# Performance work log

Hardware: AMD Instinct MI355X
Metric: run time of the kernel (lower is better)

## Reference

```python
import jax, jax.numpy as jnp
import numpy as np

INPUT_DIM = 1024
EMBED_DIMS = 128


def setup_inputs() -> dict:
    key = jax.random.key(0)
    ks = jax.random.split(key, 7)
    s_in = 1.0 / np.sqrt(INPUT_DIM)
    x = jax.random.normal(ks[0], (4, 4096, INPUT_DIM), dtype=jnp.float32)
    Wq = jax.random.uniform(ks[1], (INPUT_DIM, EMBED_DIMS), jnp.float32, -s_in, s_in)
    bq = jax.random.uniform(ks[2], (EMBED_DIMS,), jnp.float32, -s_in, s_in)
    Wk = jax.random.uniform(ks[3], (INPUT_DIM, EMBED_DIMS), jnp.float32, -s_in, s_in)
    bk = jax.random.uniform(ks[4], (EMBED_DIMS,), jnp.float32, -s_in, s_in)
    Wv = jax.random.uniform(ks[5], (INPUT_DIM, EMBED_DIMS), jnp.float32, -s_in, s_in)
    bv = jax.random.uniform(ks[6], (EMBED_DIMS,), jnp.float32, -s_in, s_in)
    return {"x": x, "Wq": Wq, "bq": bq, "Wk": Wk, "bk": bk, "Wv": Wv, "bv": bv}


def reference(x, Wq, bq, Wk, bk, Wv, bv):
    # x: [B, L, C]
    Q = jnp.einsum('blc,cd->bld', x, Wq) + bq  # [B, L, D]
    K = jnp.einsum('blc,cd->bld', x, Wk) + bk
    V = jnp.einsum('blc,cd->bld', x, Wv) + bv
    d_k = Q.shape[-1]
    scores = jnp.einsum('bld,bmd->blm', Q, K) / jnp.sqrt(jnp.float32(d_k))  # [B, L, L]
    attn = jax.nn.softmax(scores, axis=-1)
    return jnp.einsum('blm,bmd->bld', attn, V)  # [B, L, D]
```

## Files before the change

### kernel.cpp

```cpp
#include <hip/hip_runtime.h>
#include <stdint.h>

typedef __bf16 bf16;
typedef __bf16 bf16x8 __attribute__((ext_vector_type(8)));
typedef __bf16 bf16x4 __attribute__((ext_vector_type(4)));
typedef _Float16 f16;
typedef f16 f16x8 __attribute__((ext_vector_type(8)));
typedef f16 f16x4 __attribute__((ext_vector_type(4)));
typedef float f32x4 __attribute__((ext_vector_type(4)));

#define LQ    16384
#define CDIM  1024
#define DDIM  128
#define NSPLIT 4
#define QS 0.12751741f

__global__ void prep_kernel(const float* __restrict__ Wq, const float* __restrict__ Wk,
                            const float* __restrict__ Wv, const float* __restrict__ bq,
                            const float* __restrict__ bk, const float* __restrict__ bv,
                            bf16* __restrict__ Wt, float* __restrict__ bias_all) {
  int idx = blockIdx.x * 256 + threadIdx.x;
  int p = idx >> 17;
  int rem = idx & 131071;
  int k = rem >> 7, n = rem & 127;
  const float* W = (p == 0) ? Wq : (p == 1) ? Wk : Wv;
  float s = (p == 0) ? QS : 1.0f;
  Wt[(size_t)(p * 128 + n) * CDIM + k] = (bf16)(W[rem] * s);
  if (idx < 384) {
    int pp = idx >> 7, nn = idx & 127;
    const float* b = (pp == 0) ? bq : (pp == 1) ? bk : bv;
    bias_all[idx] = b[nn] * ((pp == 0) ? QS : 1.0f);
  }
}

__global__ __launch_bounds__(256, 2) void qkv_gemm(
    const float* __restrict__ x, const bf16* __restrict__ Wt,
    const float* __restrict__ bias_all,
    bf16* __restrict__ Qw, bf16* __restrict__ Kw, f16* __restrict__ Vtw) {
  __shared__ bf16 Al[2][128 * 72];
  __shared__ bf16 Bl[2][128 * 72];
  const int t = threadIdx.x;
  const int w = t >> 6;
  const int lane = t & 63;
  const int l15 = lane & 15;
  const int quad = lane >> 4;
  const int y = blockIdx.y;
  const int m0 = blockIdx.x * 128;
  const bf16* W = Wt + (size_t)y * (DDIM * CDIM);
  const int m_off = (w & 1) * 64;
  const int n_off = (w >> 1) * 64;

  f32x4 zero4 = {0.f, 0.f, 0.f, 0.f};
  f32x4 acc[4][4];
#pragma unroll
  for (int i = 0; i < 4; i++)
#pragma unroll
    for (int j = 0; j < 4; j++) acc[i][j] = zero4;

  const int xrr = t >> 4;
  const int xc = (t & 15) << 2;
  const int wr = t >> 3;
  const int wc = (t & 7) << 3;

  float4 xa[8];
  bf16x8 wa[4];
#pragma unroll
  for (int c = 0; c < 8; c++)
    xa[c] = *(const float4*)&x[(size_t)(m0 + c * 16 + xrr) * CDIM + xc];
#pragma unroll
  for (int c = 0; c < 4; c++)
    wa[c] = *(const bf16x8*)&W[(size_t)(c * 32 + wr) * CDIM + wc];

  for (int kc = 0; kc < 16; kc++) {
    bf16* Ab = Al[kc & 1];
    bf16* Bb = Bl[kc & 1];
#pragma unroll
    for (int c = 0; c < 8; c++) {
      bf16x4 v;
      v[0] = (bf16)xa[c].x; v[1] = (bf16)xa[c].y;
      v[2] = (bf16)xa[c].z; v[3] = (bf16)xa[c].w;
      *(bf16x4*)&Ab[(c * 16 + xrr) * 72 + xc] = v;
    }
#pragma unroll
    for (int c = 0; c < 4; c++)
      *(bf16x8*)&Bb[(c * 32 + wr) * 72 + wc] = wa[c];

    const int kn = (kc < 15 ? kc + 1 : 15) * 64;
#pragma unroll
    for (int c = 0; c < 8; c++)
      xa[c] = *(const float4*)&x[(size_t)(m0 + c * 16 + xrr) * CDIM + kn + xc];
#pragma unroll
    for (int c = 0; c < 4; c++)
      wa[c] = *(const bf16x8*)&W[(size_t)(c * 32 + wr) * CDIM + kn + wc];

    __syncthreads();

#pragma unroll
    for (int ks = 0; ks < 2; ks++) {
      bf16x8 af[4], bfr[4];
#pragma unroll
      for (int mt = 0; mt < 4; mt++)
        af[mt] = *(const bf16x8*)&Ab[(m_off + mt * 16 + l15) * 72 + ks * 32 + quad * 8];
#pragma unroll
      for (int nt = 0; nt < 4; nt++)
        bfr[nt] = *(const bf16x8*)&Bb[(n_off + nt * 16 + l15) * 72 + ks * 32 + quad * 8];
#pragma unroll
      for (int mt = 0; mt < 4; mt++)
#pragma unroll
        for (int nt = 0; nt < 4; nt++)
          acc[mt][nt] = __builtin_amdgcn_mfma_f32_16x16x32_bf16(af[mt], bfr[nt], acc[mt][nt], 0, 0, 0);
    }
  }

  float bias4[4];
#pragma unroll
  for (int nt = 0; nt < 4; nt++) bias4[nt] = bias_all[y * 128 + n_off + nt * 16 + l15];

  if (y < 2) {
    bf16* outp = (y == 0) ? Qw : Kw;
#pragma unroll
    for (int mt = 0; mt < 4; mt++)
#pragma unroll
      for (int nt = 0; nt < 4; nt++) {
        int n = n_off + nt * 16 + l15;
#pragma unroll
        for (int r = 0; r < 4; r++) {
          int m = m0 + m_off + mt * 16 + quad * 4 + r;
          outp[(size_t)m * DDIM + n] = (bf16)(acc[mt][nt][r] + bias4[nt]);
        }
      }
  } else {
#pragma unroll
    for (int mt = 0; mt < 4; mt++)
#pragma unroll
      for (int nt = 0; nt < 4; nt++) {
        int n = n_off + nt * 16 + l15;
        int m = m0 + m_off + mt * 16 + quad * 4;
        f16x4 pv;
#pragma unroll
        for (int r = 0; r < 4; r++) pv[r] = (f16)(acc[mt][nt][r] + bias4[nt]);
        *(f16x4*)&Vtw[(size_t)n * LQ + m] = pv;
      }
  }
}

__global__ __launch_bounds__(256, 2) void flash_kernel(
    const bf16* __restrict__ Qw, const bf16* __restrict__ Kw, const f16* __restrict__ Vtw,
    bf16* __restrict__ Opb, float* __restrict__ lp) {
  __shared__ bf16 Kl[2][64 * 136];
  __shared__ f16  Vl[2][128 * 72];

  const int t = threadIdx.x;
  const int w = t >> 6;
  const int lane = t & 63;
  const int l15 = lane & 15;
  const int quad = lane >> 4;
  const int qb = blockIdx.x;
  const int sp = blockIdx.y;
  const int batch = qb >> 5;
  const int q0w = qb * 128 + w * 32;
  const int kv_base = batch * 4096 + sp * 1024;

  bf16x8 qf[2][4];
#pragma unroll
  for (int nq = 0; nq < 2; nq++)
#pragma unroll
    for (int ks = 0; ks < 4; ks++)
      qf[nq][ks] = *(const bf16x8*)&Qw[(size_t)(q0w + nq * 16 + l15) * DDIM + ks * 32 + quad * 8];

  f32x4 zero4 = {0.f, 0.f, 0.f, 0.f};
  f32x4 o[2][8];
#pragma unroll
  for (int nq = 0; nq < 2; nq++)
#pragma unroll
    for (int dt = 0; dt < 8; dt++) o[nq][dt] = zero4;
  f32x4 li4[2];
  li4[0] = zero4; li4[1] = zero4;

  f16x4 onef = {(f16)1.f, (f16)1.f, (f16)1.f, (f16)1.f};

  const int kr = t >> 4;
  const int kcol = (t & 15) << 3;
  const int vr = t >> 3;
  const int vcol = (t & 7) << 3;

  bf16x8 ka[4];
  f16x8 va[4];
#pragma unroll
  for (int c = 0; c < 4; c++)
    ka[c] = *(const bf16x8*)&Kw[(size_t)(kv_base + c * 16 + kr) * DDIM + kcol];
#pragma unroll
  for (int c = 0; c < 4; c++)
    va[c] = *(const f16x8*)&Vtw[(size_t)(c * 32 + vr) * LQ + kv_base + vcol];

  for (int tile = 0; tile < 16; tile++) {
    bf16* Kb = Kl[tile & 1];
    f16*  Vb = Vl[tile & 1];
#pragma unroll
    for (int c = 0; c < 4; c++)
      *(bf16x8*)&Kb[(c * 16 + kr) * 136 + kcol] = ka[c];
#pragma unroll
    for (int c = 0; c < 4; c++)
      *(f16x8*)&Vb[(c * 32 + vr) * 72 + vcol] = va[c];

    const int kvn = kv_base + (tile < 15 ? tile + 1 : 15) * 64;
#pragma unroll
    for (int c = 0; c < 4; c++)
      ka[c] = *(const bf16x8*)&Kw[(size_t)(kvn + c * 16 + kr) * DDIM + kcol];
#pragma unroll
    for (int c = 0; c < 4; c++)
      va[c] = *(const f16x8*)&Vtw[(size_t)(c * 32 + vr) * LQ + kvn + vcol];

    __syncthreads();

    f32x4 sv[4][2];
#pragma unroll
    for (int mk = 0; mk < 4; mk++)
#pragma unroll
      for (int nq = 0; nq < 2; nq++) sv[mk][nq] = zero4;
#pragma unroll
    for (int ks = 0; ks < 4; ks++) {
      bf16x8 kf[4];
#pragma unroll
      for (int mk = 0; mk < 4; mk++)
        kf[mk] = *(const bf16x8*)&Kb[(mk * 16 + l15) * 136 + ks * 32 + quad * 8];
#pragma unroll
      for (int mk = 0; mk < 4; mk++)
#pragma unroll
        for (int nq = 0; nq < 2; nq++)
          sv[mk][nq] = __builtin_amdgcn_mfma_f32_16x16x32_bf16(kf[mk], qf[nq][ks], sv[mk][nq], 0, 0, 0);
    }

#pragma unroll
    for (int mk = 0; mk < 4; mk++)
#pragma unroll
      for (int nq = 0; nq < 2; nq++)
#pragma unroll
        for (int r = 0; r < 4; r++)
          sv[mk][nq][r] = exp2f(sv[mk][nq][r]);

#pragma unroll
    for (int s = 0; s < 4; s++) {
      f16x4 pa[2];
#pragma unroll
      for (int nq = 0; nq < 2; nq++) {
        f16x4 p;
#pragma unroll
        for (int r = 0; r < 4; r++) p[r] = (f16)sv[s][nq][r];
        pa[nq] = p;
      }
#pragma unroll
      for (int dt = 0; dt < 8; dt++) {
        f16x4 vf = *(const f16x4*)&Vb[(dt * 16 + l15) * 72 + s * 16 + quad * 4];
#pragma unroll
        for (int nq = 0; nq < 2; nq++)
          o[nq][dt] = __builtin_amdgcn_mfma_f32_16x16x16f16(pa[nq], vf, o[nq][dt], 0, 0, 0);
      }
#pragma unroll
      for (int nq = 0; nq < 2; nq++)
        li4[nq] = __builtin_amdgcn_mfma_f32_16x16x16f16(pa[nq], onef, li4[nq], 0, 0, 0);
    }
  }

  const size_t po = (size_t)sp * LQ * DDIM;
#pragma unroll
  for (int nq = 0; nq < 2; nq++)
#pragma unroll
    for (int dt = 0; dt < 8; dt++)
#pragma unroll
      for (int r = 0; r < 4; r++)
        Opb[po + (size_t)(q0w + nq * 16 + quad * 4 + r) * DDIM + dt * 16 + l15] = (bf16)o[nq][dt][r];
  if (l15 == 0) {
#pragma unroll
    for (int nq = 0; nq < 2; nq++)
#pragma unroll
      for (int r = 0; r < 4; r++)
        lp[(size_t)sp * LQ + q0w + nq * 16 + quad * 4 + r] = li4[nq][r];
  }
}

__global__ void combine_kernel(const bf16* __restrict__ Opb, const float* __restrict__ lp,
                               float* __restrict__ out) {
  int idx = blockIdx.x * 256 + threadIdx.x;
  int q = idx >> 5;
  int d = (idx & 31) * 4;
  float lsum = 0.f;
  float acc[4] = {0.f, 0.f, 0.f, 0.f};
#pragma unroll
  for (int sp = 0; sp < NSPLIT; sp++) {
    lsum += lp[(size_t)sp * LQ + q];
    bf16x4 ov = *(const bf16x4*)&Opb[(size_t)sp * LQ * DDIM + (size_t)q * DDIM + d];
#pragma unroll
    for (int j = 0; j < 4; j++) acc[j] += (float)ov[j];
  }
  float inv = 1.0f / lsum;
  float4 r;
  r.x = acc[0] * inv; r.y = acc[1] * inv; r.z = acc[2] * inv; r.w = acc[3] * inv;
  *(float4*)&out[(size_t)q * DDIM + d] = r;
}

extern "C" void kernel_launch(void* const* d_in, const int* in_sizes, int n_in,
                              void* d_out, int out_size, void* d_ws, size_t ws_size,
                              hipStream_t stream) {
  const float* x  = (const float*)d_in[0];
  const float* Wq = (const float*)d_in[1];
  const float* bq = (const float*)d_in[2];
  const float* Wk = (const float*)d_in[3];
  const float* bk = (const float*)d_in[4];
  const float* Wv = (const float*)d_in[5];
  const float* bv = (const float*)d_in[6];
  char* ws = (char*)d_ws;
  bf16* Qw   = (bf16*)(ws);
  bf16* Kw   = (bf16*)(ws + ((size_t)4 << 20));
  f16*  Vtw  = (f16*)(ws + ((size_t)8 << 20));
  bf16* Wt   = (bf16*)(ws + ((size_t)12 << 20));
  float* bias_all = (float*)(ws + ((size_t)12 << 20) + 786432);
  bf16* Opb  = (bf16*)(ws + ((size_t)13 << 20));
  float* lpp = (float*)(ws + ((size_t)29 << 20));
  float* out = (float*)d_out;

  prep_kernel<<<1536, 256, 0, stream>>>(Wq, Wk, Wv, bq, bk, bv, Wt, bias_all);
  qkv_gemm<<<dim3(128, 3), 256, 0, stream>>>(x, Wt, bias_all, Qw, Kw, Vtw);
  flash_kernel<<<dim3(128, NSPLIT), 256, 0, stream>>>(Qw, Kw, Vtw, Opb, lpp);
  combine_kernel<<<2048, 256, 0, stream>>>(Opb, lpp, out);
}
```

Measured before the change: 182.8 us.

## Shrink QKV GEMM tile, read K directly from global, store partials as fp16

After: 208.1 us. 1.14x slower.

```diff
diff --git a/kernel.cpp b/kernel.cpp
--- a/kernel.cpp
+++ b/kernel.cpp
@@ -33,79 +33,76 @@
   }
 }
 
-__global__ __launch_bounds__(256, 2) void qkv_gemm(
+__global__ __launch_bounds__(256, 3) void qkv_gemm(
     const float* __restrict__ x, const bf16* __restrict__ Wt,
     const float* __restrict__ bias_all,
     bf16* __restrict__ Qw, bf16* __restrict__ Kw, f16* __restrict__ Vtw) {
-  __shared__ bf16 Al[2][128 * 72];
-  __shared__ bf16 Bl[2][128 * 72];
+  __shared__ bf16 Al[64 * 72];
+  __shared__ bf16 Bl[128 * 72];
   const int t = threadIdx.x;
   const int w = t >> 6;
   const int lane = t & 63;
   const int l15 = lane & 15;
   const int quad = lane >> 4;
   const int y = blockIdx.y;
-  const int m0 = blockIdx.x * 128;
+  const int m0 = blockIdx.x * 64;
   const bf16* W = Wt + (size_t)y * (DDIM * CDIM);
-  const int m_off = (w & 1) * 64;
+  const int m_off = (w & 1) * 32;
   const int n_off = (w >> 1) * 64;
-
-  f32x4 zero4 = {0.f, 0.f, 0.f, 0.f};
-  f32x4 acc[4][4];
-#pragma unroll
-  for (int i = 0; i < 4; i++)
-#pragma unroll
-    for (int j = 0; j < 4; j++) acc[i][j] = zero4;
-
-  const int xrr = t >> 4;
+  const int xr = t >> 4;
   const int xc = (t & 15) << 2;
   const int wr = t >> 3;
   const int wc = (t & 7) << 3;
 
-  float4 xa[8];
+  f32x4 zero4 = {0.f, 0.f, 0.f, 0.f};
+  f32x4 acc[2][4];
+#pragma unroll
+  for (int i = 0; i < 2; i++)
+#pragma unroll
+    for (int j = 0; j < 4; j++) acc[i][j] = zero4;
+
+  float4 xa[4];
   bf16x8 wa[4];
 #pragma unroll
-  for (int c = 0; c < 8; c++)
-    xa[c] = *(const float4*)&x[(size_t)(m0 + c * 16 + xrr) * CDIM + xc];
+  for (int c = 0; c < 4; c++)
+    xa[c] = *(const float4*)&x[(size_t)(m0 + c * 16 + xr) * CDIM + xc];
 #pragma unroll
   for (int c = 0; c < 4; c++)
     wa[c] = *(const bf16x8*)&W[(size_t)(c * 32 + wr) * CDIM + wc];
 
   for (int kc = 0; kc < 16; kc++) {
-    bf16* Ab = Al[kc & 1];
-    bf16* Bb = Bl[kc & 1];
-#pragma unroll
-    for (int c = 0; c < 8; c++) {
+    __syncthreads();
+#pragma unroll
+    for (int c = 0; c < 4; c++) {
       bf16x4 v;
       v[0] = (bf16)xa[c].x; v[1] = (bf16)xa[c].y;
       v[2] = (bf16)xa[c].z; v[3] = (bf16)xa[c].w;
-      *(bf16x4*)&Ab[(c * 16 + xrr) * 72 + xc] = v;
+      *(bf16x4*)&Al[(c * 16 + xr) * 72 + xc] = v;
     }
 #pragma unroll
     for (int c = 0; c < 4; c++)
-      *(bf16x8*)&Bb[(c * 32 + wr) * 72 + wc] = wa[c];
+      *(bf16x8*)&Bl[(c * 32 + wr) * 72 + wc] = wa[c];
+    __syncthreads();
 
     const int kn = (kc < 15 ? kc + 1 : 15) * 64;
 #pragma unroll
-    for (int c = 0; c < 8; c++)
-      xa[c] = *(const float4*)&x[(size_t)(m0 + c * 16 + xrr) * CDIM + kn + xc];
+    for (int c = 0; c < 4; c++)
+      xa[c] = *(const float4*)&x[(size_t)(m0 + c * 16 + xr) * CDIM + kn + xc];
 #pragma unroll
     for (int c = 0; c < 4; c++)
       wa[c] = *(const bf16x8*)&W[(size_t)(c * 32 + wr) * CDIM + kn + wc];
 
-    __syncthreads();
-
 #pragma unroll
     for (int ks = 0; ks < 2; ks++) {
-      bf16x8 af[4], bfr[4];
-#pragma unroll
-      for (int mt = 0; mt < 4; mt++)
-        af[mt] = *(const bf16x8*)&Ab[(m_off + mt * 16 + l15) * 72 + ks * 32 + quad * 8];
+      bf16x8 af[2], bfr[4];
+#pragma unroll
+      for (int mt = 0; mt < 2; mt++)
+        af[mt] = *(const bf16x8*)&Al[(m_off + mt * 16 + l15) * 72 + ks * 32 + quad * 8];
 #pragma unroll
       for (int nt = 0; nt < 4; nt++)
-        bfr[nt] = *(const bf16x8*)&Bb[(n_off + nt * 16 + l15) * 72 + ks * 32 + quad * 8];
-#pragma unroll
-      for (int mt = 0; mt < 4; mt++)
+        bfr[nt] = *(const bf16x8*)&Bl[(n_off + nt * 16 + l15) * 72 + ks * 32 + quad * 8];
+#pragma unroll
+      for (int mt = 0; mt < 2; mt++)
 #pragma unroll
         for (int nt = 0; nt < 4; nt++)
           acc[mt][nt] = __builtin_amdgcn_mfma_f32_16x16x32_bf16(af[mt], bfr[nt], acc[mt][nt], 0, 0, 0);
@@ -119,7 +116,7 @@
   if (y < 2) {
     bf16* outp = (y == 0) ? Qw : Kw;
 #pragma unroll
-    for (int mt = 0; mt < 4; mt++)
+    for (int mt = 0; mt < 2; mt++)
 #pragma unroll
       for (int nt = 0; nt < 4; nt++) {
         int n = n_off + nt * 16 + l15;
@@ -131,7 +128,7 @@
       }
   } else {
 #pragma unroll
-    for (int mt = 0; mt < 4; mt++)
+    for (int mt = 0; mt < 2; mt++)
 #pragma unroll
       for (int nt = 0; nt < 4; nt++) {
         int n = n_off + nt * 16 + l15;
@@ -146,9 +143,8 @@
 
 __global__ __launch_bounds__(256, 2) void flash_kernel(
     const bf16* __restrict__ Qw, const bf16* __restrict__ Kw, const f16* __restrict__ Vtw,
-    bf16* __restrict__ Opb, float* __restrict__ lp) {
-  __shared__ bf16 Kl[2][64 * 136];
-  __shared__ f16  Vl[2][128 * 72];
+    f16* __restrict__ Opb, float* __restrict__ lp) {
+  __shared__ f16 Vl[2][128 * 72];
 
   const int t = threadIdx.x;
   const int w = t >> 6;
@@ -179,26 +175,17 @@
 
   f16x4 onef = {(f16)1.f, (f16)1.f, (f16)1.f, (f16)1.f};
 
-  const int kr = t >> 4;
-  const int kcol = (t & 15) << 3;
   const int vr = t >> 3;
   const int vcol = (t & 7) << 3;
 
-  bf16x8 ka[4];
   f16x8 va[4];
-#pragma unroll
-  for (int c = 0; c < 4; c++)
-    ka[c] = *(const bf16x8*)&Kw[(size_t)(kv_base + c * 16 + kr) * DDIM + kcol];
 #pragma unroll
   for (int c = 0; c < 4; c++)
     va[c] = *(const f16x8*)&Vtw[(size_t)(c * 32 + vr) * LQ + kv_base + vcol];
 
   for (int tile = 0; tile < 16; tile++) {
-    bf16* Kb = Kl[tile & 1];
-    f16*  Vb = Vl[tile & 1];
-#pragma unroll
-    for (int c = 0; c < 4; c++)
-      *(bf16x8*)&Kb[(c * 16 + kr) * 136 + kcol] = ka[c];
+    const int kv0 = kv_base + tile * 64;
+    f16* Vb = Vl[tile & 1];
 #pragma unroll
     for (int c = 0; c < 4; c++)
       *(f16x8*)&Vb[(c * 32 + vr) * 72 + vcol] = va[c];
@@ -206,49 +193,34 @@
     const int kvn = kv_base + (tile < 15 ? tile + 1 : 15) * 64;
 #pragma unroll
     for (int c = 0; c < 4; c++)
-      ka[c] = *(const bf16x8*)&Kw[(size_t)(kvn + c * 16 + kr) * DDIM + kcol];
-#pragma unroll
-    for (int c = 0; c < 4; c++)
       va[c] = *(const f16x8*)&Vtw[(size_t)(c * 32 + vr) * LQ + kvn + vcol];
 
     __syncthreads();
 
-    f32x4 sv[4][2];
-#pragma unroll
-    for (int mk = 0; mk < 4; mk++)
-#pragma unroll
-      for (int nq = 0; nq < 2; nq++) sv[mk][nq] = zero4;
-#pragma unroll
-    for (int ks = 0; ks < 4; ks++) {
+#pragma unroll
+    for (int s = 0; s < 4; s++) {
       bf16x8 kf[4];
 #pragma unroll
-      for (int mk = 0; mk < 4; mk++)
-        kf[mk] = *(const bf16x8*)&Kb[(mk * 16 + l15) * 136 + ks * 32 + quad * 8];
-#pragma unroll
-      for (int mk = 0; mk < 4; mk++)
+      for (int ks = 0; ks < 4; ks++)
+        kf[ks] = *(const bf16x8*)&Kw[(size_t)(kv0 + s * 16 + l15) * DDIM + ks * 32 + quad * 8];
+
+      f32x4 sv[2];
+      sv[0] = zero4; sv[1] = zero4;
+#pragma unroll
+      for (int ks = 0; ks < 4; ks++)
 #pragma unroll
         for (int nq = 0; nq < 2; nq++)
-          sv[mk][nq] = __builtin_amdgcn_mfma_f32_16x16x32_bf16(kf[mk], qf[nq][ks], sv[mk][nq], 0, 0, 0);
-    }
-
-#pragma unroll
-    for (int mk = 0; mk < 4; mk++)
-#pragma unroll
-      for (int nq = 0; nq < 2; nq++)
-#pragma unroll
-        for (int r = 0; r < 4; r++)
-          sv[mk][nq][r] = exp2f(sv[mk][nq][r]);
-
-#pragma unroll
-    for (int s = 0; s < 4; s++) {
+          sv[nq] = __builtin_amdgcn_mfma_f32_16x16x32_bf16(kf[ks], qf[nq][ks], sv[nq], 0, 0, 0);
+
       f16x4 pa[2];
 #pragma unroll
       for (int nq = 0; nq < 2; nq++) {
         f16x4 p;
 #pragma unroll
-        for (int r = 0; r < 4; r++) p[r] = (f16)sv[s][nq][r];
+        for (int r = 0; r < 4; r++) p[r] = (f16)exp2f(sv[nq][r]);
         pa[nq] = p;
       }
+
 #pragma unroll
       for (int dt = 0; dt < 8; dt++) {
         f16x4 vf = *(const f16x4*)&Vb[(dt * 16 + l15) * 72 + s * 16 + quad * 4];
@@ -269,7 +241,7 @@
     for (int dt = 0; dt < 8; dt++)
 #pragma unroll
       for (int r = 0; r < 4; r++)
-        Opb[po + (size_t)(q0w + nq * 16 + quad * 4 + r) * DDIM + dt * 16 + l15] = (bf16)o[nq][dt][r];
+        Opb[po + (size_t)(q0w + nq * 16 + quad * 4 + r) * DDIM + dt * 16 + l15] = (f16)o[nq][dt][r];
   if (l15 == 0) {
 #pragma unroll
     for (int nq = 0; nq < 2; nq++)
@@ -279,7 +251,7 @@
   }
 }
 
-__global__ void combine_kernel(const bf16* __restrict__ Opb, const float* __restrict__ lp,
+__global__ void combine_kernel(const f16* __restrict__ Opb, const float* __restrict__ lp,
                                float* __restrict__ out) {
   int idx = blockIdx.x * 256 + threadIdx.x;
   int q = idx >> 5;
@@ -289,7 +261,7 @@
 #pragma unroll
   for (int sp = 0; sp < NSPLIT; sp++) {
     lsum += lp[(size_t)sp * LQ + q];
-    bf16x4 ov = *(const bf16x4*)&Opb[(size_t)sp * LQ * DDIM + (size_t)q * DDIM + d];
+    f16x4 ov = *(const f16x4*)&Opb[(size_t)sp * LQ * DDIM + (size_t)q * DDIM + d];
 #pragma unroll
     for (int j = 0; j < 4; j++) acc[j] += (float)ov[j];
   }
@@ -315,12 +287,12 @@
   f16*  Vtw  = (f16*)(ws + ((size_t)8 << 20));
   bf16* Wt   = (bf16*)(ws + ((size_t)12 << 20));
   float* bias_all = (float*)(ws + ((size_t)12 << 20) + 786432);
-  bf16* Opb  = (bf16*)(ws + ((size_t)13 << 20));
+  f16*  Opb  = (f16*)(ws + ((size_t)13 << 20));
   float* lpp = (float*)(ws + ((size_t)29 << 20));
   float* out = (float*)d_out;
 
   prep_kernel<<<1536, 256, 0, stream>>>(Wq, Wk, Wv, bq, bk, bv, Wt, bias_all);
-  qkv_gemm<<<dim3(128, 3), 256, 0, stream>>>(x, Wt, bias_all, Qw, Kw, Vtw);
+  qkv_gemm<<<dim3(256, 3), 256, 0, stream>>>(x, Wt, bias_all, Qw, Kw, Vtw);
   flash_kernel<<<dim3(128, NSPLIT), 256, 0, stream>>>(Qw, Kw, Vtw, Opb, lpp);
   combine_kernel<<<2048, 256, 0, stream>>>(Opb, lpp, out);
 }
```
